# Kernel tuning notes

Hardware: AMD Instinct MI355X
Metric: run time of the kernel (lower is better)

Reference implementation:

```python
import jax, jax.numpy as jnp
import numpy as np

N, C, D = 16384, 10000, 128
LR = 0.5


def setup_inputs() -> dict:
    key = jax.random.key(0)
    k1, k2, k3 = jax.random.split(key, 3)
    embeded_preds = jax.random.normal(k1, (N, D), dtype=jnp.float32)
    idx = jax.random.randint(k2, (N,), 0, C)
    labels = jax.nn.one_hot(idx, C, dtype=jnp.float32)  # [N, C] one-hot, as the TF layer expects
    center = jax.random.normal(k3, (C, D), dtype=jnp.float32) * 0.02
    return {"embeded_preds": embeded_preds, "labels": labels, "center": center}


def reference(embeded_preds, labels, center):
    # gather: per-sample class center via one-hot matmul  [N, C] @ [C, D] -> [N, D]
    embeded_labels = jnp.matmul(labels, center)
    diff = embeded_labels - embeded_preds  # [N, D]
    # scatter-add: accumulate diffs per class  [C, N] @ [N, D] -> [C, D]
    grad = jnp.matmul(labels.T, diff)
    center_counts = jnp.sum(labels.T, axis=1, keepdims=True) + 1.0  # [C, 1]
    grad = grad / center_counts
    updated_center = center - LR * grad  # value assigned back to the center variable
    return updated_center
```

## Files before the change

### kernel.cpp

```cpp
#include <hip/hip_runtime.h>
#include <hip/hip_bf16.h>

#define N_SAMPLES 16384
#define N_CLASSES 10000
#define DIM 128
#define LR_CONST 0.5f

__global__ __launch_bounds__(256) void gather_scatter_kernel(
    const float* __restrict__ labels,
    const float* __restrict__ preds,
    const float* __restrict__ center,
    float* __restrict__ grad,
    int* __restrict__ counts)
{
    const int n = blockIdx.x;
    __shared__ int s_class;

    const float4* row = reinterpret_cast<const float4*>(labels + (size_t)n * N_CLASSES);
    const int nvec = N_CLASSES / 4;
    for (int j = threadIdx.x; j < nvec; j += blockDim.x) {
        float4 v = row[j];
        int c = -1;
        if (v.x > 0.5f)      c = 4 * j + 0;
        else if (v.y > 0.5f) c = 4 * j + 1;
        else if (v.z > 0.5f) c = 4 * j + 2;
        else if (v.w > 0.5f) c = 4 * j + 3;
        if (c >= 0) s_class = c;
    }
    __syncthreads();
    const int c = s_class;

    if (threadIdx.x == 0) {
        atomicAdd(&counts[c], 1);
    }
    if (threadIdx.x < DIM) {
        const int d = threadIdx.x;
        float diff = center[(size_t)c * DIM + d] - preds[(size_t)n * DIM + d];
        atomicAdd(&grad[(size_t)c * DIM + d], diff);
    }
}

__global__ __launch_bounds__(256) void finalize_kernel(
    const float* __restrict__ center,
    const float* __restrict__ grad,
    const int* __restrict__ counts,
    float* __restrict__ out)
{
    int t = blockIdx.x * blockDim.x + threadIdx.x;
    if (t >= N_CLASSES * DIM) return;
    int c = t >> 7;
    float cnt = (float)counts[c] + 1.0f;
    out[t] = center[t] - LR_CONST * (grad[t] / cnt);
}

extern "C" void kernel_launch(void* const* d_in, const int* in_sizes, int n_in,
                              void* d_out, int out_size, void* d_ws, size_t ws_size,
                              hipStream_t stream) {
    const float* preds  = (const float*)d_in[0];
    const float* labels = (const float*)d_in[1];
    const float* center = (const float*)d_in[2];
    float* out = (float*)d_out;

    float* grad  = (float*)d_ws;
    int*   counts = (int*)((char*)d_ws + (size_t)N_CLASSES * DIM * sizeof(float));
    size_t zero_bytes = (size_t)N_CLASSES * DIM * sizeof(float) + (size_t)N_CLASSES * sizeof(int);

    hipMemsetAsync(d_ws, 0, zero_bytes, stream);

    gather_scatter_kernel<<<N_SAMPLES, 256, 0, stream>>>(labels, preds, center, grad, counts);

    const int total = N_CLASSES * DIM;
    finalize_kernel<<<(total + 255) / 256, 256, 0, stream>>>(center, grad, counts, out);
}
```

Measured before the change: 860.8 us.

## Scan one-hot rows per wavefront with ballot-based early exit

New measurement: 770.4 us. 1.12x faster.

```diff
diff --git a/kernel.cpp b/kernel.cpp
--- a/kernel.cpp
+++ b/kernel.cpp
@@ -6,6 +6,8 @@
 #define DIM 128
 #define LR_CONST 0.5f
 
+typedef float f32x4 __attribute__((ext_vector_type(4)));
+
 __global__ __launch_bounds__(256) void gather_scatter_kernel(
     const float* __restrict__ labels,
     const float* __restrict__ preds,
@@ -13,31 +15,46 @@
     float* __restrict__ grad,
     int* __restrict__ counts)
 {
-    const int n = blockIdx.x;
-    __shared__ int s_class;
+    const int lane = threadIdx.x & 63;
+    const int n = blockIdx.x * 4 + (threadIdx.x >> 6);
 
-    const float4* row = reinterpret_cast<const float4*>(labels + (size_t)n * N_CLASSES);
+    const f32x4* row = reinterpret_cast<const f32x4*>(labels + (size_t)n * N_CLASSES);
     const int nvec = N_CLASSES / 4;
-    for (int j = threadIdx.x; j < nvec; j += blockDim.x) {
-        float4 v = row[j];
-        int c = -1;
-        if (v.x > 0.5f)      c = 4 * j + 0;
-        else if (v.y > 0.5f) c = 4 * j + 1;
-        else if (v.z > 0.5f) c = 4 * j + 2;
-        else if (v.w > 0.5f) c = 4 * j + 3;
-        if (c >= 0) s_class = c;
+
+    int c = -1;
+    for (int cb = 0; cb < nvec; cb += 128) {
+        const int j0 = cb + lane;
+        const int j1 = cb + 64 + lane;
+        f32x4 v0 = (f32x4)(0.0f);
+        f32x4 v1 = (f32x4)(0.0f);
+        if (j0 < nvec) v0 = __builtin_nontemporal_load(row + j0);
+        if (j1 < nvec) v1 = __builtin_nontemporal_load(row + j1);
+
+        int local = -1;
+        if      (v0.x > 0.5f) local = 4 * j0 + 0;
+        else if (v0.y > 0.5f) local = 4 * j0 + 1;
+        else if (v0.z > 0.5f) local = 4 * j0 + 2;
+        else if (v0.w > 0.5f) local = 4 * j0 + 3;
+        else if (v1.x > 0.5f) local = 4 * j1 + 0;
+        else if (v1.y > 0.5f) local = 4 * j1 + 1;
+        else if (v1.z > 0.5f) local = 4 * j1 + 2;
+        else if (v1.w > 0.5f) local = 4 * j1 + 3;
+
+        unsigned long long m = __ballot(local >= 0);
+        if (m) {
+            const int src = __ffsll((unsigned long long)m) - 1;
+            c = __shfl(local, src);
+            break;
+        }
     }
-    __syncthreads();
-    const int c = s_class;
 
-    if (threadIdx.x == 0) {
-        atomicAdd(&counts[c], 1);
-    }
-    if (threadIdx.x < DIM) {
-        const int d = threadIdx.x;
-        float diff = center[(size_t)c * DIM + d] - preds[(size_t)n * DIM + d];
-        atomicAdd(&grad[(size_t)c * DIM + d], diff);
-    }
+    if (lane == 0) atomicAdd(&counts[c], 1);
+    const size_t cb128 = (size_t)c * DIM;
+    const size_t nb128 = (size_t)n * DIM;
+    const float d0 = center[cb128 + lane]      - preds[nb128 + lane];
+    const float d1 = center[cb128 + lane + 64] - preds[nb128 + lane + 64];
+    atomicAdd(&grad[cb128 + lane], d0);
+    atomicAdd(&grad[cb128 + lane + 64], d1);
 }
 
 __global__ __launch_bounds__(256) void finalize_kernel(
@@ -50,7 +67,8 @@
     if (t >= N_CLASSES * DIM) return;
     int c = t >> 7;
     float cnt = (float)counts[c] + 1.0f;
-    out[t] = center[t] - LR_CONST * (grad[t] / cnt);
+    float v = center[t] - LR_CONST * (grad[t] / cnt);
+    __builtin_nontemporal_store(v, out + t);
 }
 
 extern "C" void kernel_launch(void* const* d_in, const int* in_sizes, int n_in,
@@ -61,13 +79,13 @@
     const float* center = (const float*)d_in[2];
     float* out = (float*)d_out;
 
-    float* grad  = (float*)d_ws;
+    float* grad   = (float*)d_ws;
     int*   counts = (int*)((char*)d_ws + (size_t)N_CLASSES * DIM * sizeof(float));
     size_t zero_bytes = (size_t)N_CLASSES * DIM * sizeof(float) + (size_t)N_CLASSES * sizeof(int);
 
     hipMemsetAsync(d_ws, 0, zero_bytes, stream);
 
-    gather_scatter_kernel<<<N_SAMPLES, 256, 0, stream>>>(labels, preds, center, grad, counts);
+    gather_scatter_kernel<<<N_SAMPLES / 4, 256, 0, stream>>>(labels, preds, center, grad, counts);
 
     const int total = N_CLASSES * DIM;
     finalize_kernel<<<(total + 255) / 256, 256, 0, stream>>>(center, grad, counts, out);
```

## Use persistent work-stealing waves with early-exit one-hot row scan

Applied to the files above, without the earlier changes.

Result: slower. 1.082 ms (+25.7%).

```diff
diff --git a/kernel.cpp b/kernel.cpp
--- a/kernel.cpp
+++ b/kernel.cpp
@@ -5,38 +5,108 @@
 #define N_CLASSES 10000
 #define DIM 128
 #define LR_CONST 0.5f
+#define NVEC 2500
+#define CHUNK 128
+
+typedef float f32x4 __attribute__((ext_vector_type(4)));
+
+__device__ __forceinline__ int wave_steal(int* counter, int lane) {
+    int r = 0;
+    if (lane == 0) r = atomicAdd(counter, 1);
+    return __shfl(r, 0);
+}
+
+__device__ __forceinline__ int test_hit(f32x4 a, int ja, f32x4 b, int jb) {
+    int local = -1;
+    if      (a.x > 0.5f) local = 4 * ja + 0;
+    else if (a.y > 0.5f) local = 4 * ja + 1;
+    else if (a.z > 0.5f) local = 4 * ja + 2;
+    else if (a.w > 0.5f) local = 4 * ja + 3;
+    else if (b.x > 0.5f) local = 4 * jb + 0;
+    else if (b.y > 0.5f) local = 4 * jb + 1;
+    else if (b.z > 0.5f) local = 4 * jb + 2;
+    else if (b.w > 0.5f) local = 4 * jb + 3;
+    return local;
+}
+
+__device__ __forceinline__ void scatter(int n, int c, int lane,
+                                        const float* __restrict__ preds,
+                                        const float* __restrict__ center,
+                                        float* __restrict__ grad,
+                                        int* __restrict__ counts) {
+    const size_t cb = (size_t)c * DIM;
+    const size_t nb = (size_t)n * DIM;
+    const float d0 = center[cb + lane]      - preds[nb + lane];
+    const float d1 = center[cb + 64 + lane] - preds[nb + 64 + lane];
+    atomicAdd(&grad[cb + lane], d0);
+    atomicAdd(&grad[cb + 64 + lane], d1);
+    if (lane == 0) atomicAdd(&counts[c], 1);
+}
 
 __global__ __launch_bounds__(256) void gather_scatter_kernel(
     const float* __restrict__ labels,
     const float* __restrict__ preds,
     const float* __restrict__ center,
     float* __restrict__ grad,
-    int* __restrict__ counts)
+    int* __restrict__ counts,
+    int* __restrict__ counter)
 {
-    const int n = blockIdx.x;
-    __shared__ int s_class;
+    const int lane = threadIdx.x & 63;
 
-    const float4* row = reinterpret_cast<const float4*>(labels + (size_t)n * N_CLASSES);
-    const int nvec = N_CLASSES / 4;
-    for (int j = threadIdx.x; j < nvec; j += blockDim.x) {
-        float4 v = row[j];
-        int c = -1;
-        if (v.x > 0.5f)      c = 4 * j + 0;
-        else if (v.y > 0.5f) c = 4 * j + 1;
-        else if (v.z > 0.5f) c = 4 * j + 2;
-        else if (v.w > 0.5f) c = 4 * j + 3;
-        if (c >= 0) s_class = c;
-    }
-    __syncthreads();
-    const int c = s_class;
+    int n0 = wave_steal(counter, lane);
+    int n1 = wave_steal(counter, lane);
+    bool a0 = n0 < N_SAMPLES;
+    bool a1 = n1 < N_SAMPLES;
+    int o0 = 0, o1 = 0;
 
-    if (threadIdx.x == 0) {
-        atomicAdd(&counts[c], 1);
-    }
-    if (threadIdx.x < DIM) {
-        const int d = threadIdx.x;
-        float diff = center[(size_t)c * DIM + d] - preds[(size_t)n * DIM + d];
-        atomicAdd(&grad[(size_t)c * DIM + d], diff);
+    while (a0 | a1) {
+        f32x4 u0 = (f32x4)(0.0f), w0 = (f32x4)(0.0f);
+        f32x4 u1 = (f32x4)(0.0f), w1 = (f32x4)(0.0f);
+        int j00 = 0, j01 = 0, j10 = 0, j11 = 0;
+
+        if (a0) {
+            const f32x4* r = reinterpret_cast<const f32x4*>(labels + (size_t)n0 * N_CLASSES);
+            j00 = o0 + lane;      if (j00 > NVEC - 1) j00 = NVEC - 1;
+            j01 = o0 + 64 + lane; if (j01 > NVEC - 1) j01 = NVEC - 1;
+            u0 = __builtin_nontemporal_load(r + j00);
+            w0 = __builtin_nontemporal_load(r + j01);
+        }
+        if (a1) {
+            const f32x4* r = reinterpret_cast<const f32x4*>(labels + (size_t)n1 * N_CLASSES);
+            j10 = o1 + lane;      if (j10 > NVEC - 1) j10 = NVEC - 1;
+            j11 = o1 + 64 + lane; if (j11 > NVEC - 1) j11 = NVEC - 1;
+            u1 = __builtin_nontemporal_load(r + j10);
+            w1 = __builtin_nontemporal_load(r + j11);
+        }
+
+        if (a0) {
+            const int local = test_hit(u0, j00, w0, j01);
+            const unsigned long long m = __ballot(local >= 0);
+            if (m) {
+                const int c = __shfl(local, __ffsll((unsigned long long)m) - 1);
+                scatter(n0, c, lane, preds, center, grad, counts);
+                n0 = wave_steal(counter, lane);
+                a0 = n0 < N_SAMPLES;
+                o0 = 0;
+            } else {
+                o0 += CHUNK;
+                if (o0 >= NVEC) a0 = false;
+            }
+        }
+        if (a1) {
+            const int local = test_hit(u1, j10, w1, j11);
+            const unsigned long long m = __ballot(local >= 0);
+            if (m) {
+                const int c = __shfl(local, __ffsll((unsigned long long)m) - 1);
+                scatter(n1, c, lane, preds, center, grad, counts);
+                n1 = wave_steal(counter, lane);
+                a1 = n1 < N_SAMPLES;
+                o1 = 0;
+            } else {
+                o1 += CHUNK;
+                if (o1 >= NVEC) a1 = false;
+            }
+        }
     }
 }
 
@@ -50,7 +120,8 @@
     if (t >= N_CLASSES * DIM) return;
     int c = t >> 7;
     float cnt = (float)counts[c] + 1.0f;
-    out[t] = center[t] - LR_CONST * (grad[t] / cnt);
+    float v = center[t] - LR_CONST * (grad[t] / cnt);
+    __builtin_nontemporal_store(v, out + t);
 }
 
 extern "C" void kernel_launch(void* const* d_in, const int* in_sizes, int n_in,
@@ -61,13 +132,15 @@
     const float* center = (const float*)d_in[2];
     float* out = (float*)d_out;
 
-    float* grad  = (float*)d_ws;
-    int*   counts = (int*)((char*)d_ws + (size_t)N_CLASSES * DIM * sizeof(float));
-    size_t zero_bytes = (size_t)N_CLASSES * DIM * sizeof(float) + (size_t)N_CLASSES * sizeof(int);
+    float* grad    = (float*)d_ws;
+    int*   counts  = (int*)((char*)d_ws + (size_t)N_CLASSES * DIM * sizeof(float));
+    int*   counter = counts + N_CLASSES;
+    size_t zero_bytes = (size_t)N_CLASSES * DIM * sizeof(float)
+                      + (size_t)N_CLASSES * sizeof(int) + sizeof(int);
 
     hipMemsetAsync(d_ws, 0, zero_bytes, stream);
 
-    gather_scatter_kernel<<<N_SAMPLES, 256, 0, stream>>>(labels, preds, center, grad, counts);
+    gather_scatter_kernel<<<2048, 256, 0, stream>>>(labels, preds, center, grad, counts, counter);
 
     const int total = N_CLASSES * DIM;
     finalize_kernel<<<(total + 255) / 256, 256, 0, stream>>>(center, grad, counts, out);
```
